# Kernel optimization log

Measured on AMD Instinct MI355X. Metric: run time of the kernel, lower is better.

## Reference

```python
import jax, jax.numpy as jnp
import numpy as np

N_NODES = 200000
N_EDGES = 600000
EMB = 128
HID = 128
N_RELS = 64
N_MOTIFS = 512
N_CENTERS = 256
N_NODE_CLASSES = 16


def _linear_params(key, out_dim, in_dim):
    kw, kb = jax.random.split(key)
    s = 1.0 / np.sqrt(in_dim)
    w = jax.random.uniform(kw, (out_dim, in_dim), jnp.float32, -s, s)
    b = jax.random.uniform(kb, (out_dim,), jnp.float32, -s, s)
    return w, b


def setup_inputs() -> dict:
    key = jax.random.key(0)
    ks = jax.random.split(key, 12)
    lin_w, lin_b = _linear_params(ks[2], HID, EMB)
    conv1_w, conv1_b = _linear_params(ks[3], HID, HID)
    conv2_w, conv2_b = _linear_params(ks[4], HID, HID)
    edge_w, edge_b = _linear_params(ks[5], N_RELS, 2 * HID)
    motif_w, motif_b = _linear_params(ks[6], N_MOTIFS, HID)
    node_w, node_b = _linear_params(ks[7], N_NODE_CLASSES, HID)
    return {
        "node_emb": jax.random.normal(ks[0], (N_NODES, EMB), jnp.float32),
        "rel_emb": jax.random.normal(ks[1], (N_RELS, EMB), jnp.float32),
        "lin_w": lin_w, "lin_b": lin_b,
        "conv1_w": conv1_w, "conv1_b": conv1_b,
        "conv2_w": conv2_w, "conv2_b": conv2_b,
        "edge_w": edge_w, "edge_b": edge_b,
        "motif_w": motif_w, "motif_b": motif_b,
        "node_w": node_w, "node_b": node_b,
        "node_ids": jnp.arange(N_NODES, dtype=jnp.int32),
        "rel_ids": jax.random.randint(ks[8], (N_EDGES,), 0, N_RELS, jnp.int32),
        "center_mol_idx": jax.random.randint(ks[9], (N_CENTERS,), 0, N_NODES, jnp.int32),
        "edge_index": jax.random.randint(ks[10], (2, N_EDGES), 0, N_NODES, jnp.int32),
    }


def _gine_conv(x, edge_index, edge_attr, w, b):
    # PyG GINEConv (eps=0): nn((1+eps)*x + sum_j relu(x_j + e_ji))
    src, dst = edge_index[0], edge_index[1]
    msg = jax.nn.relu(x[src] + edge_attr)               # [E, H]
    agg = jax.ops.segment_sum(msg, dst, num_segments=x.shape[0])  # [N, H]
    return (agg + x) @ w.T + b


def reference(node_emb, rel_emb, lin_w, lin_b, conv1_w, conv1_b,
              conv2_w, conv2_b, edge_w, edge_b, motif_w, motif_b,
              node_w, node_b, node_ids, rel_ids, center_mol_idx, edge_index):
    x = node_emb[node_ids]            # [N, EMB]
    edge_attr = rel_emb[rel_ids]      # [E, EMB]
    x = x @ lin_w.T + lin_b           # [N, H]
    edge_attr = edge_attr @ lin_w.T + lin_b  # [E, H]
    x = _gine_conv(x, edge_index, edge_attr, conv1_w, conv1_b)
    x = jax.nn.relu(x)
    x = _gine_conv(x, edge_index, edge_attr, conv2_w, conv2_b)
    edge_pred_input = jnp.concatenate([x[edge_index[0]], x[edge_index[1]]], axis=1)  # [E, 2H]
    edge_class = edge_pred_input @ edge_w.T + edge_b       # [E, num_rels]
    center = x[center_mol_idx]                             # [C, H]
    motif_pred = center @ motif_w.T + motif_b              # [C, num_motifs]
    node_class = x @ node_w.T + node_b                     # [N, 16]
    return (edge_class, motif_pred, node_class)
```

## Files before the change

kernel.cpp:

```cpp
#include <hip/hip_runtime.h>
#include <hip/hip_bf16.h>

#define N_NODES 200000
#define N_EDGES 600000
#define EMB 128
#define HID 128
#define N_RELS 64
#define N_MOTIFS 512
#define N_CENTERS 256
#define NCLS 16

#define SCAN_C 512
#define NB_SCAN ((N_NODES + SCAN_C - 1) / SCAN_C)

typedef unsigned short u16;
typedef __attribute__((ext_vector_type(8))) short short8;
typedef __attribute__((ext_vector_type(4))) float f32x4;

__device__ __forceinline__ float bf2f(u16 u) {
    unsigned int i = ((unsigned int)u) << 16;
    float f; __builtin_memcpy(&f, &i, 4); return f;
}
__device__ __forceinline__ u16 f2bf(float f) {
    unsigned int x; __builtin_memcpy(&x, &f, 4);
    x += 0x7fffu + ((x >> 16) & 1u);
    return (u16)(x >> 16);
}

#define O_LINW   0
#define O_LINB   16384
#define O_C1W    16512
#define O_C1B    32896
#define O_C2W    33024
#define O_C2B    49408
#define O_EW     49536
#define O_EB     65920
#define O_MW     65984
#define O_MB     131520
#define O_NW     132032
#define O_NB     134080
#define N_WB     134096

__global__ void k_cvt(const float* __restrict__ lw, const float* __restrict__ lb,
                      const float* __restrict__ c1w, const float* __restrict__ c1b,
                      const float* __restrict__ c2w, const float* __restrict__ c2b,
                      const float* __restrict__ ew, const float* __restrict__ eb,
                      const float* __restrict__ mw, const float* __restrict__ mb,
                      const float* __restrict__ nw, const float* __restrict__ nb,
                      u16* __restrict__ wb)
{
    const int t = blockIdx.x * 256 + threadIdx.x;
    if (t >= N_WB) return;
    float v;
    if      (t < O_LINB) v = lw[t - O_LINW];
    else if (t < O_C1W)  v = lb[t - O_LINB];
    else if (t < O_C1B)  v = c1w[t - O_C1W];
    else if (t < O_C2W)  v = c1b[t - O_C1B];
    else if (t < O_C2B)  v = c2w[t - O_C2W];
    else if (t < O_EW)   v = c2b[t - O_C2B];
    else if (t < O_EB)   v = ew[t - O_EW];
    else if (t < O_MW)   v = eb[t - O_EB];
    else if (t < O_MB)   v = mw[t - O_MW];
    else if (t < O_NW)   v = mb[t - O_MB];
    else if (t < O_NB)   v = nw[t - O_NW];
    else                 v = nb[t - O_NB];
    wb[t] = f2bf(v);
}

__global__ void k_rel(const float* __restrict__ rel_emb, const float* __restrict__ lw,
                      const float* __restrict__ lb, float* __restrict__ rel_lin)
{
    __shared__ float e[EMB];
    const int r = blockIdx.x, h = threadIdx.x;
    e[h] = rel_emb[r * EMB + h];
    __syncthreads();
    const float* wr = lw + (size_t)h * EMB;
    float acc = lb[h];
    #pragma unroll
    for (int k0 = 0; k0 < EMB; k0 += 4) {
        f32x4 wv = *(const f32x4*)(wr + k0);
        #pragma unroll
        for (int j = 0; j < 4; ++j) acc += e[k0 + j] * wv[j];
    }
    rel_lin[r * HID + h] = acc;
}

__global__ void k_hist(const int* __restrict__ dst, int* __restrict__ deg)
{
    const int e = blockIdx.x * 256 + threadIdx.x;
    if (e < N_EDGES) atomicAdd(&deg[dst[e]], 1);
}

__global__ void k_scan1(const int* __restrict__ deg, int* __restrict__ bsum)
{
    __shared__ int sd[256];
    const int t = threadIdx.x, base = blockIdx.x * SCAN_C;
    int v = 0;
    int i0 = base + t, i1 = base + 256 + t;
    if (i0 < N_NODES) v += deg[i0];
    if (i1 < N_NODES) v += deg[i1];
    sd[t] = v; __syncthreads();
    for (int s = 128; s > 0; s >>= 1) {
        if (t < s) sd[t] += sd[t + s];
        __syncthreads();
    }
    if (t == 0) bsum[blockIdx.x] = sd[0];
}

__global__ void k_scan2(int* __restrict__ bsum, int* __restrict__ row_ptr)
{
    __shared__ int sh[512];
    const int t = threadIdx.x;
    int v = (t < NB_SCAN) ? bsum[t] : 0;
    sh[t] = v;
    for (int off = 1; off < 512; off <<= 1) {
        __syncthreads();
        int a = (t >= off) ? sh[t - off] : 0;
        __syncthreads();
        sh[t] += a;
    }
    __syncthreads();
    if (t < NB_SCAN) bsum[t] = sh[t] - v;
    if (t == 511) row_ptr[N_NODES] = sh[511];
}

__global__ void k_scan3(const int* __restrict__ deg, const int* __restrict__ bsum,
                        int* __restrict__ row_ptr)
{
    __shared__ int sh[256];
    const int t = threadIdx.x, base = blockIdx.x * SCAN_C;
    const int i0 = base + 2 * t, i1 = i0 + 1;
    int d0 = (i0 < N_NODES) ? deg[i0] : 0;
    int d1 = (i1 < N_NODES) ? deg[i1] : 0;
    int p = d0 + d1;
    sh[t] = p;
    for (int off = 1; off < 256; off <<= 1) {
        __syncthreads();
        int a = (t >= off) ? sh[t - off] : 0;
        __syncthreads();
        sh[t] += a;
    }
    __syncthreads();
    const int off = bsum[blockIdx.x] + sh[t] - p;
    if (i0 < N_NODES) row_ptr[i0] = off;
    if (i1 < N_NODES) row_ptr[i1] = off + d0;
}

__global__ void k_fill(const int* __restrict__ src, const int* __restrict__ dst,
                       const int* __restrict__ rid, const int* __restrict__ row_ptr,
                       int* __restrict__ cur, int* __restrict__ srcrid)
{
    const int e = blockIdx.x * 256 + threadIdx.x;
    if (e >= N_EDGES) return;
    const int d = dst[e];
    const int pos = row_ptr[d] + atomicAdd(&cur[d], 1);
    srcrid[pos] = src[e] * 64 + rid[e];
}

__global__ __launch_bounds__(256) void k_lin(
    const float* __restrict__ emb, const int* __restrict__ ids,
    const u16* __restrict__ w, const u16* __restrict__ bias,
    u16* __restrict__ out)
{
    const int wid = threadIdx.x >> 6, lane = threadIdx.x & 63;
    const int r15 = lane & 15, kg = (lane >> 4) * 8;
    const int arow = blockIdx.x * 64 + wid * 16 + r15;
    const int srow = ids[arow];
    const float* ar = emb + (size_t)srow * EMB + kg;
    short8 a[4];
    #pragma unroll
    for (int kk = 0; kk < 4; ++kk) {
        f32x4 a0 = *(const f32x4*)(ar + kk * 32);
        f32x4 a1 = *(const f32x4*)(ar + kk * 32 + 4);
        short8 t;
        #pragma unroll
        for (int j = 0; j < 4; ++j) { t[j] = (short)f2bf(a0[j]); t[4 + j] = (short)f2bf(a1[j]); }
        a[kk] = t;
    }
    f32x4 acc[8];
    #pragma unroll
    for (int nb = 0; nb < 8; ++nb) acc[nb] = (f32x4){0.f, 0.f, 0.f, 0.f};
    #pragma unroll
    for (int nb = 0; nb < 8; ++nb) {
        const u16* wr = w + (size_t)(nb * 16 + r15) * EMB + kg;
        #pragma unroll
        for (int kk = 0; kk < 4; ++kk) {
            short8 bv = *(const short8*)(wr + kk * 32);
            acc[nb] = __builtin_amdgcn_mfma_f32_16x16x32_bf16(a[kk], bv, acc[nb], 0, 0, 0);
        }
    }
    const int ob = blockIdx.x * 64 + wid * 16 + (lane >> 4) * 4;
    #pragma unroll
    for (int nb = 0; nb < 8; ++nb) {
        const int col = nb * 16 + r15;
        const float bn = bf2f(bias[col]);
        #pragma unroll
        for (int r = 0; r < 4; ++r)
            out[(size_t)(ob + r) * HID + col] = f2bf(acc[nb][r] + bn);
    }
}

#define ALD 136
__global__ __launch_bounds__(256) void k_fuse(
    const u16* __restrict__ x, const float* __restrict__ rel_lin,
    const int* __restrict__ row_ptr, const int* __restrict__ srcrid,
    const u16* __restrict__ w, const u16* __restrict__ bias,
    u16* __restrict__ out, const int do_relu)
{
    __shared__ u16 atile[64 * ALD];

    const int nl = threadIdx.x >> 2;
    const int n = blockIdx.x * 64 + nl;
    const int q = (threadIdx.x & 3) * 32;
    const int pbeg = row_ptr[n], pend = row_ptr[n + 1];

    float acc[32];
    #pragma unroll
    for (int j = 0; j < 32; ++j) acc[j] = 0.f;

    int p = pbeg;
    for (; p + 2 <= pend; p += 2) {
        const int v0 = srcrid[p], v1 = srcrid[p + 1];
        const int s0 = v0 >> 6, r0 = v0 & 63;
        const int s1 = v1 >> 6, r1 = v1 & 63;
        const u16* xp0 = x + (size_t)s0 * HID + q;
        const u16* xp1 = x + (size_t)s1 * HID + q;
        const float* rp0 = rel_lin + r0 * HID + q;
        const float* rp1 = rel_lin + r1 * HID + q;
        short8 xv0[4], xv1[4];
        f32x4 rv0[8], rv1[8];
        #pragma unroll
        for (int c = 0; c < 4; ++c) { xv0[c] = *(const short8*)(xp0 + c * 8);
                                      xv1[c] = *(const short8*)(xp1 + c * 8); }
        #pragma unroll
        for (int c = 0; c < 8; ++c) { rv0[c] = *(const f32x4*)(rp0 + c * 4);
                                      rv1[c] = *(const f32x4*)(rp1 + c * 4); }
        #pragma unroll
        for (int c = 0; c < 4; ++c)
            #pragma unroll
            for (int j = 0; j < 8; ++j) {
                acc[c * 8 + j] += fmaxf(bf2f((u16)xv0[c][j]) + rv0[c * 2 + (j >> 2)][j & 3], 0.f);
                acc[c * 8 + j] += fmaxf(bf2f((u16)xv1[c][j]) + rv1[c * 2 + (j >> 2)][j & 3], 0.f);
            }
    }
    if (p < pend) {
        const int v = srcrid[p];
        const int s = v >> 6, r = v & 63;
        const u16* xp = x + (size_t)s * HID + q;
        const float* rp = rel_lin + r * HID + q;
        #pragma unroll
        for (int c = 0; c < 4; ++c) {
            short8 xv = *(const short8*)(xp + c * 8);
            #pragma unroll
            for (int j = 0; j < 8; ++j)
                acc[c * 8 + j] += fmaxf(bf2f((u16)xv[j]) + rp[c * 8 + j], 0.f);
        }
    }
    {
        const u16* xp = x + (size_t)n * HID + q;
        #pragma unroll
        for (int c = 0; c < 4; ++c) {
            short8 xv = *(const short8*)(xp + c * 8);
            short8 t;
            #pragma unroll
            for (int j = 0; j < 8; ++j) t[j] = (short)f2bf(acc[c * 8 + j] + bf2f((u16)xv[j]));
            *(short8*)(&atile[nl * ALD + q + c * 8]) = t;
        }
    }
    __syncthreads();

    const int wid = threadIdx.x >> 6, lane = threadIdx.x & 63;
    const int r15 = lane & 15, kg = (lane >> 4) * 8;
    const int lrow = wid * 16 + r15;
    short8 a[4];
    #pragma unroll
    for (int kk = 0; kk < 4; ++kk) a[kk] = *(const short8*)(&atile[lrow * ALD + kg + kk * 32]);
    f32x4 accm[8];
    #pragma unroll
    for (int nb = 0; nb < 8; ++nb) accm[nb] = (f32x4){0.f, 0.f, 0.f, 0.f};
    #pragma unroll
    for (int nb = 0; nb < 8; ++nb) {
        const u16* wr = w + (size_t)(nb * 16 + r15) * HID + kg;
        #pragma unroll
        for (int kk = 0; kk < 4; ++kk) {
            short8 bv = *(const short8*)(wr + kk * 32);
            accm[nb] = __builtin_amdgcn_mfma_f32_16x16x32_bf16(a[kk], bv, accm[nb], 0, 0, 0);
        }
    }
    const int ob = blockIdx.x * 64 + wid * 16 + (lane >> 4) * 4;
    #pragma unroll
    for (int nb = 0; nb < 8; ++nb) {
        const int col = nb * 16 + r15;
        const float bn = bf2f(bias[col]);
        #pragma unroll
        for (int r = 0; r < 4; ++r) {
            float v = accm[nb][r] + bn;
            if (do_relu) v = fmaxf(v, 0.f);
            out[(size_t)(ob + r) * HID + col] = f2bf(v);
        }
    }
}

__global__ __launch_bounds__(256) void k_heads(
    const u16* __restrict__ x2, const u16* __restrict__ ew,
    const u16* __restrict__ nw, const u16* __restrict__ nbias,
    u16* __restrict__ y, float* __restrict__ node_out)
{
    const int wid = threadIdx.x >> 6, lane = threadIdx.x & 63;
    const int r15 = lane & 15, kg = (lane >> 4) * 8;
    const int arow = blockIdx.x * 64 + wid * 16 + r15;
    const u16* xr = x2 + (size_t)arow * HID + kg;
    short8 a[4];
    #pragma unroll
    for (int kk = 0; kk < 4; ++kk) a[kk] = *(const short8*)(xr + kk * 32);

    f32x4 accs[4], accd[4], accn;
    #pragma unroll
    for (int nb = 0; nb < 4; ++nb) {
        accs[nb] = (f32x4){0.f, 0.f, 0.f, 0.f};
        accd[nb] = (f32x4){0.f, 0.f, 0.f, 0.f};
    }
    accn = (f32x4){0.f, 0.f, 0.f, 0.f};

    #pragma unroll
    for (int nb = 0; nb < 4; ++nb) {
        const u16* wr = ew + (size_t)(nb * 16 + r15) * 256 + kg;
        #pragma unroll
        for (int kk = 0; kk < 4; ++kk) {
            short8 bs = *(const short8*)(wr + kk * 32);
            short8 bd = *(const short8*)(wr + 128 + kk * 32);
            accs[nb] = __builtin_amdgcn_mfma_f32_16x16x32_bf16(a[kk], bs, accs[nb], 0, 0, 0);
            accd[nb] = __builtin_amdgcn_mfma_f32_16x16x32_bf16(a[kk], bd, accd[nb], 0, 0, 0);
        }
    }
    {
        const u16* wr = nw + (size_t)r15 * HID + kg;
        #pragma unroll
        for (int kk = 0; kk < 4; ++kk) {
            short8 bv = *(const short8*)(wr + kk * 32);
            accn = __builtin_amdgcn_mfma_f32_16x16x32_bf16(a[kk], bv, accn, 0, 0, 0);
        }
    }

    const int ob = blockIdx.x * 64 + wid * 16 + (lane >> 4) * 4;
    #pragma unroll
    for (int nb = 0; nb < 4; ++nb) {
        const int col = nb * 16 + r15;
        #pragma unroll
        for (int r = 0; r < 4; ++r) {
            y[(size_t)(ob + r) * 128 + col] = f2bf(accs[nb][r]);
            y[(size_t)(ob + r) * 128 + 64 + col] = f2bf(accd[nb][r]);
        }
    }
    const float bn = bf2f(nbias[r15]);
    #pragma unroll
    for (int r = 0; r < 4; ++r)
        node_out[(size_t)(ob + r) * NCLS + r15] = accn[r] + bn;
}

__global__ __launch_bounds__(256) void k_eout(
    const u16* __restrict__ y, const int* __restrict__ src, const int* __restrict__ dst,
    const float* __restrict__ eb, float* __restrict__ out)
{
    const int t = blockIdx.x * 256 + threadIdx.x;
    const int e = t >> 2;
    const int qq = (t & 3) * 16;
    const int s = src[e], d = dst[e];
    const u16* ys = y + (size_t)s * 128 + qq;
    const u16* yd = y + (size_t)d * 128 + 64 + qq;
    const float* ebp = eb + qq;
    float* op = out + (size_t)e * 64 + qq;
    #pragma unroll
    for (int c = 0; c < 2; ++c) {
        short8 vs = *(const short8*)(ys + c * 8);
        short8 vd = *(const short8*)(yd + c * 8);
        #pragma unroll
        for (int h = 0; h < 2; ++h) {
            f32x4 vb = *(const f32x4*)(ebp + c * 8 + h * 4);
            f32x4 r;
            #pragma unroll
            for (int j = 0; j < 4; ++j)
                r[j] = bf2f((u16)vs[h * 4 + j]) + bf2f((u16)vd[h * 4 + j]) + vb[j];
            *(f32x4*)(op + c * 8 + h * 4) = r;
        }
    }
}

__global__ void k_motif(const u16* __restrict__ x2, const int* __restrict__ centers,
                        const u16* __restrict__ mw, const u16* __restrict__ mb,
                        float* __restrict__ out)
{
    __shared__ float xs[HID];
    const int c = blockIdx.x, m = threadIdx.x;
    if (m < HID) xs[m] = bf2f(x2[(size_t)centers[c] * HID + m]);
    __syncthreads();
    const u16* wr = mw + (size_t)m * HID;
    float acc = bf2f(mb[m]);
    #pragma unroll
    for (int k0 = 0; k0 < HID; k0 += 8) {
        short8 wv = *(const short8*)(wr + k0);
        #pragma unroll
        for (int j = 0; j < 8; ++j) acc += xs[k0 + j] * bf2f((u16)wv[j]);
    }
    out[(size_t)c * N_MOTIFS + m] = acc;
}

extern "C" void kernel_launch(void* const* d_in, const int* in_sizes, int n_in,
                              void* d_out, int out_size, void* d_ws, size_t ws_size,
                              hipStream_t stream)
{
    const float* node_emb = (const float*)d_in[0];
    const float* rel_emb  = (const float*)d_in[1];
    const float* lin_w    = (const float*)d_in[2];
    const float* lin_b    = (const float*)d_in[3];
    const float* conv1_w  = (const float*)d_in[4];
    const float* conv1_b  = (const float*)d_in[5];
    const float* conv2_w  = (const float*)d_in[6];
    const float* conv2_b  = (const float*)d_in[7];
    const float* edge_w   = (const float*)d_in[8];
    const float* edge_b   = (const float*)d_in[9];
    const float* motif_w  = (const float*)d_in[10];
    const float* motif_b  = (const float*)d_in[11];
    const float* node_w   = (const float*)d_in[12];
    const float* node_b   = (const float*)d_in[13];
    const int* node_ids = (const int*)d_in[14];
    const int* rel_ids  = (const int*)d_in[15];
    const int* centers  = (const int*)d_in[16];
    const int* src      = (const int*)d_in[17];
    const int* dst      = ((const int*)d_in[17]) + N_EDGES;

    char* ws = (char*)d_ws;
    float* rel_lin = (float*)ws;
    u16*   wb      = (u16*)(ws + 32768);
    u16*   x0      = (u16*)(ws + 524288);
    u16*   x1      = (u16*)(ws + 524288 + 51200000);
    u16*   y       = (u16*)(ws + 524288 + 2 * 51200000);
    char*  csr     = ws + 524288 + 2 * 51200000 + 102400000;
    int*   deg     = (int*)csr;
    int*   cur     = (int*)(csr + 800000);
    int*   row_ptr = (int*)(csr + 1600000);
    int*   srcrid  = (int*)(csr + 2400032);
    int*   bsum    = (int*)(csr + 4800032);
    u16*   x2      = x0;

    float* out_edge  = (float*)d_out;
    float* out_motif = out_edge + (size_t)N_EDGES * 64;
    float* out_node  = out_motif + (size_t)N_CENTERS * N_MOTIFS;

    k_cvt<<<(N_WB + 255) / 256, 256, 0, stream>>>(
        lin_w, lin_b, conv1_w, conv1_b, conv2_w, conv2_b,
        edge_w, edge_b, motif_w, motif_b, node_w, node_b, wb);
    hipMemsetAsync(deg, 0, 1600000, stream);
    k_rel<<<N_RELS, 128, 0, stream>>>(rel_emb, lin_w, lin_b, rel_lin);

    k_hist<<<(N_EDGES + 255) / 256, 256, 0, stream>>>(dst, deg);
    k_scan1<<<NB_SCAN, 256, 0, stream>>>(deg, bsum);
    k_scan2<<<1, 512, 0, stream>>>(bsum, row_ptr);
    k_scan3<<<NB_SCAN, 256, 0, stream>>>(deg, bsum, row_ptr);
    k_fill<<<(N_EDGES + 255) / 256, 256, 0, stream>>>(src, dst, rel_ids, row_ptr, cur, srcrid);

    k_lin<<<N_NODES / 64, 256, 0, stream>>>(node_emb, node_ids, wb + O_LINW, wb + O_LINB, x0);
    k_fuse<<<N_NODES / 64, 256, 0, stream>>>(x0, rel_lin, row_ptr, srcrid,
                                             wb + O_C1W, wb + O_C1B, x1, 1);
    k_fuse<<<N_NODES / 64, 256, 0, stream>>>(x1, rel_lin, row_ptr, srcrid,
                                             wb + O_C2W, wb + O_C2B, x2, 0);
    k_heads<<<N_NODES / 64, 256, 0, stream>>>(x2, wb + O_EW, wb + O_NW, wb + O_NB, y, out_node);
    k_eout<<<(N_EDGES * 4) / 256, 256, 0, stream>>>(y, src, dst, edge_b, out_edge);
    k_motif<<<N_CENTERS, N_MOTIFS, 0, stream>>>(x2, centers, wb + O_MW, wb + O_MB, out_motif);
}
```

Before: 541.0 us.

## Gather in MFMA lane layout with LDS-cached bf16 relation table

The two small prep kernels (weight bf16 conversion and relation linear) are merged into one launch. In the GINE fused kernel, each lane now aggregates neighbor messages directly in the MFMA A-operand layout, which removes the shared-memory staging tile and a block barrier. The relation embeddings are cached per block in LDS as bf16 with an XOR swizzle rather than read as fp32 from global memory. The costs are an LDS fill per block, an extra rounding of the relation values to bf16, and a different per-thread gather pattern in which 16-byte chunks are strided by 32 elements.

```diff
diff --git a/kernel.cpp b/kernel.cpp
--- a/kernel.cpp
+++ b/kernel.cpp
@@ -41,15 +41,32 @@
 #define O_NB     134080
 #define N_WB     134096
 
-__global__ void k_cvt(const float* __restrict__ lw, const float* __restrict__ lb,
+__global__ void k_pre(const float* __restrict__ rel_emb,
+                      const float* __restrict__ lw, const float* __restrict__ lb,
                       const float* __restrict__ c1w, const float* __restrict__ c1b,
                       const float* __restrict__ c2w, const float* __restrict__ c2b,
                       const float* __restrict__ ew, const float* __restrict__ eb,
                       const float* __restrict__ mw, const float* __restrict__ mb,
                       const float* __restrict__ nw, const float* __restrict__ nb,
-                      u16* __restrict__ wb)
-{
-    const int t = blockIdx.x * 256 + threadIdx.x;
+                      float* __restrict__ rel_lin, u16* __restrict__ wb)
+{
+    if (blockIdx.x < 64) {
+        __shared__ float e[EMB];
+        const int r = blockIdx.x, h = threadIdx.x;
+        e[h] = rel_emb[r * EMB + h];
+        __syncthreads();
+        const float* wr = lw + (size_t)h * EMB;
+        float acc = lb[h];
+        #pragma unroll
+        for (int k0 = 0; k0 < EMB; k0 += 4) {
+            f32x4 wv = *(const f32x4*)(wr + k0);
+            #pragma unroll
+            for (int j = 0; j < 4; ++j) acc += e[k0 + j] * wv[j];
+        }
+        rel_lin[r * HID + h] = acc;
+        return;
+    }
+    const int t = (blockIdx.x - 64) * 128 + threadIdx.x;
     if (t >= N_WB) return;
     float v;
     if      (t < O_LINB) v = lw[t - O_LINW];
@@ -67,24 +84,6 @@
     wb[t] = f2bf(v);
 }
 
-__global__ void k_rel(const float* __restrict__ rel_emb, const float* __restrict__ lw,
-                      const float* __restrict__ lb, float* __restrict__ rel_lin)
-{
-    __shared__ float e[EMB];
-    const int r = blockIdx.x, h = threadIdx.x;
-    e[h] = rel_emb[r * EMB + h];
-    __syncthreads();
-    const float* wr = lw + (size_t)h * EMB;
-    float acc = lb[h];
-    #pragma unroll
-    for (int k0 = 0; k0 < EMB; k0 += 4) {
-        f32x4 wv = *(const f32x4*)(wr + k0);
-        #pragma unroll
-        for (int j = 0; j < 4; ++j) acc += e[k0 + j] * wv[j];
-    }
-    rel_lin[r * HID + h] = acc;
-}
-
 __global__ void k_hist(const int* __restrict__ dst, int* __restrict__ deg)
 {
     const int e = blockIdx.x * 256 + threadIdx.x;
@@ -200,18 +199,32 @@
     }
 }
 
-#define ALD 136
 __global__ __launch_bounds__(256) void k_fuse(
     const u16* __restrict__ x, const float* __restrict__ rel_lin,
     const int* __restrict__ row_ptr, const int* __restrict__ srcrid,
     const u16* __restrict__ w, const u16* __restrict__ bias,
     u16* __restrict__ out, const int do_relu)
 {
-    __shared__ u16 atile[64 * ALD];
-
-    const int nl = threadIdx.x >> 2;
-    const int n = blockIdx.x * 64 + nl;
-    const int q = (threadIdx.x & 3) * 32;
+    __shared__ u16 rel[N_RELS * 128];
+    {
+        const int r = threadIdx.x >> 2;
+        #pragma unroll
+        for (int k = 0; k < 4; ++k) {
+            const int ch = (threadIdx.x & 3) * 4 + k;
+            const float* sp = rel_lin + r * HID + ch * 8;
+            short8 t;
+            #pragma unroll
+            for (int j = 0; j < 8; ++j) t[j] = (short)f2bf(sp[j]);
+            *(short8*)(&rel[r * 128 + ((ch ^ (r & 7)) * 8)]) = t;
+        }
+    }
+    __syncthreads();
+
+    const int wid = threadIdx.x >> 6, lane = threadIdx.x & 63;
+    const int r15 = lane & 15;
+    const int kq  = lane >> 4;
+    const int kg  = kq * 8;
+    const int n = blockIdx.x * 64 + wid * 16 + r15;
     const int pbeg = row_ptr[n], pend = row_ptr[n + 1];
 
     float acc[32];
@@ -223,58 +236,51 @@
         const int v0 = srcrid[p], v1 = srcrid[p + 1];
         const int s0 = v0 >> 6, r0 = v0 & 63;
         const int s1 = v1 >> 6, r1 = v1 & 63;
-        const u16* xp0 = x + (size_t)s0 * HID + q;
-        const u16* xp1 = x + (size_t)s1 * HID + q;
-        const float* rp0 = rel_lin + r0 * HID + q;
-        const float* rp1 = rel_lin + r1 * HID + q;
-        short8 xv0[4], xv1[4];
-        f32x4 rv0[8], rv1[8];
-        #pragma unroll
-        for (int c = 0; c < 4; ++c) { xv0[c] = *(const short8*)(xp0 + c * 8);
-                                      xv1[c] = *(const short8*)(xp1 + c * 8); }
-        #pragma unroll
-        for (int c = 0; c < 8; ++c) { rv0[c] = *(const f32x4*)(rp0 + c * 4);
-                                      rv1[c] = *(const f32x4*)(rp1 + c * 4); }
-        #pragma unroll
-        for (int c = 0; c < 4; ++c)
+        const u16* xp0 = x + (size_t)s0 * HID + kg;
+        const u16* xp1 = x + (size_t)s1 * HID + kg;
+        short8 xv0[4], xv1[4], rv0[4], rv1[4];
+        #pragma unroll
+        for (int kk = 0; kk < 4; ++kk) {
+            xv0[kk] = *(const short8*)(xp0 + kk * 32);
+            xv1[kk] = *(const short8*)(xp1 + kk * 32);
+            rv0[kk] = *(const short8*)(&rel[r0 * 128 + (((kq + kk * 4) ^ (r0 & 7)) * 8)]);
+            rv1[kk] = *(const short8*)(&rel[r1 * 128 + (((kq + kk * 4) ^ (r1 & 7)) * 8)]);
+        }
+        #pragma unroll
+        for (int kk = 0; kk < 4; ++kk)
             #pragma unroll
             for (int j = 0; j < 8; ++j) {
-                acc[c * 8 + j] += fmaxf(bf2f((u16)xv0[c][j]) + rv0[c * 2 + (j >> 2)][j & 3], 0.f);
-                acc[c * 8 + j] += fmaxf(bf2f((u16)xv1[c][j]) + rv1[c * 2 + (j >> 2)][j & 3], 0.f);
+                acc[kk * 8 + j] += fmaxf(bf2f((u16)xv0[kk][j]) + bf2f((u16)rv0[kk][j]), 0.f);
+                acc[kk * 8 + j] += fmaxf(bf2f((u16)xv1[kk][j]) + bf2f((u16)rv1[kk][j]), 0.f);
             }
     }
     if (p < pend) {
         const int v = srcrid[p];
         const int s = v >> 6, r = v & 63;
-        const u16* xp = x + (size_t)s * HID + q;
-        const float* rp = rel_lin + r * HID + q;
-        #pragma unroll
-        for (int c = 0; c < 4; ++c) {
-            short8 xv = *(const short8*)(xp + c * 8);
+        const u16* xp = x + (size_t)s * HID + kg;
+        #pragma unroll
+        for (int kk = 0; kk < 4; ++kk) {
+            short8 xv = *(const short8*)(xp + kk * 32);
+            short8 rv = *(const short8*)(&rel[r * 128 + (((kq + kk * 4) ^ (r & 7)) * 8)]);
             #pragma unroll
             for (int j = 0; j < 8; ++j)
-                acc[c * 8 + j] += fmaxf(bf2f((u16)xv[j]) + rp[c * 8 + j], 0.f);
-        }
-    }
+                acc[kk * 8 + j] += fmaxf(bf2f((u16)xv[j]) + bf2f((u16)rv[j]), 0.f);
+        }
+    }
+
+    short8 a[4];
     {
-        const u16* xp = x + (size_t)n * HID + q;
-        #pragma unroll
-        for (int c = 0; c < 4; ++c) {
-            short8 xv = *(const short8*)(xp + c * 8);
+        const u16* xp = x + (size_t)n * HID + kg;
+        #pragma unroll
+        for (int kk = 0; kk < 4; ++kk) {
+            short8 xv = *(const short8*)(xp + kk * 32);
             short8 t;
             #pragma unroll
-            for (int j = 0; j < 8; ++j) t[j] = (short)f2bf(acc[c * 8 + j] + bf2f((u16)xv[j]));
-            *(short8*)(&atile[nl * ALD + q + c * 8]) = t;
-        }
-    }
-    __syncthreads();
-
-    const int wid = threadIdx.x >> 6, lane = threadIdx.x & 63;
-    const int r15 = lane & 15, kg = (lane >> 4) * 8;
-    const int lrow = wid * 16 + r15;
-    short8 a[4];
-    #pragma unroll
-    for (int kk = 0; kk < 4; ++kk) a[kk] = *(const short8*)(&atile[lrow * ALD + kg + kk * 32]);
+            for (int j = 0; j < 8; ++j) t[j] = (short)f2bf(acc[kk * 8 + j] + bf2f((u16)xv[j]));
+            a[kk] = t;
+        }
+    }
+
     f32x4 accm[8];
     #pragma unroll
     for (int nb = 0; nb < 8; ++nb) accm[nb] = (f32x4){0.f, 0.f, 0.f, 0.f};
@@ -447,11 +453,10 @@
     float* out_motif = out_edge + (size_t)N_EDGES * 64;
     float* out_node  = out_motif + (size_t)N_CENTERS * N_MOTIFS;
 
-    k_cvt<<<(N_WB + 255) / 256, 256, 0, stream>>>(
-        lin_w, lin_b, conv1_w, conv1_b, conv2_w, conv2_b,
-        edge_w, edge_b, motif_w, motif_b, node_w, node_b, wb);
+    k_pre<<<64 + (N_WB + 127) / 128, 128, 0, stream>>>(
+        rel_emb, lin_w, lin_b, conv1_w, conv1_b, conv2_w, conv2_b,
+        edge_w, edge_b, motif_w, motif_b, node_w, node_b, rel_lin, wb);
     hipMemsetAsync(deg, 0, 1600000, stream);
-    k_rel<<<N_RELS, 128, 0, stream>>>(rel_emb, lin_w, lin_b, rel_lin);
 
     k_hist<<<(N_EDGES + 255) / 256, 256, 0, stream>>>(dst, deg);
     k_scan1<<<NB_SCAN, 256, 0, stream>>>(deg, bsum);
```

Result: faster. 469.6 us (-13.2%).
